# Optimization experiments

Measured on AMD Instinct MI355X. Metric: run time of the kernel, lower is better.

## Reference

```python
import jax, jax.numpy as jnp
import numpy as np

N = 50000          # total residues (nodes)
E = 800000         # contact edges
IN_DIM = 1280      # ESM embedding dim
G_DIMS = [512, 512, 512]
FC0, FC1 = 1024, 512
OUT = 256
N_GRAPHS = 64


def setup_inputs() -> dict:
    key = jax.random.key(0)
    ks = jax.random.split(key, 16)
    inp = {
        "x": jax.random.normal(ks[0], (N, IN_DIM), dtype=jnp.float32),
        "edge_index": jax.random.randint(ks[1], (2, E), 0, N, dtype=jnp.int64),
        "batch": jnp.sort(jax.random.randint(ks[2], (N,), 0, N_GRAPHS, dtype=jnp.int64)),
    }
    s = 0.02
    dims = [IN_DIM] + G_DIMS
    for i in range(3):
        inp[f"Wg{i+1}"] = jax.random.normal(ks[3 + i], (dims[i], dims[i + 1]), dtype=jnp.float32) * s
        inp[f"bg{i+1}"] = jnp.zeros((dims[i + 1],), dtype=jnp.float32)
    cat = sum(G_DIMS)  # 1536
    inp["Wr"] = jax.random.normal(ks[7], (cat, FC0), dtype=jnp.float32) * s
    inp["br"] = jnp.zeros((FC0,), dtype=jnp.float32)
    inp["Wf"] = jax.random.normal(ks[8], (FC0, FC1), dtype=jnp.float32) * s
    inp["bf"] = jnp.zeros((FC1,), dtype=jnp.float32)
    inp["Wo"] = jax.random.normal(ks[9], (FC1, OUT), dtype=jnp.float32) * s
    inp["bo"] = jnp.zeros((OUT,), dtype=jnp.float32)
    return inp


def _gcn_layer(x, W, b, src, dst, n):
    # PyG GCNConv: h = X W; add self loops; symmetric deg^-1/2 normalization; sum-aggregate; + bias
    h = x @ W                                    # [n, d_out]
    ones = jnp.ones_like(src, dtype=h.dtype)
    deg = jax.ops.segment_sum(ones, dst, num_segments=n) + 1.0   # in-degree incl. self loop
    dinv = jax.lax.rsqrt(deg)
    norm = dinv[src] * dinv[dst]                 # [E]
    agg = jax.ops.segment_sum(h[src] * norm[:, None], dst, num_segments=n)
    agg = agg + h * (dinv * dinv)[:, None]       # self-loop contribution: 1/deg
    return agg + b


def reference(x, edge_index, batch, Wg1, bg1, Wg2, bg2, Wg3, bg3, Wr, br, Wf, bf, Wo, bo):
    n = x.shape[0]
    src, dst = edge_index[0], edge_index[1]
    h1 = _gcn_layer(x, Wg1, bg1, src, dst, n)
    h2 = _gcn_layer(h1, Wg2, bg2, src, dst, n)
    h3 = _gcn_layer(h2, Wg3, bg3, src, dst, n)
    h = jnp.concatenate([h1, h2, h3], axis=-1)   # [n, 1536]
    # global mean pool per graph
    s = jax.ops.segment_sum(h, batch, num_segments=N_GRAPHS)
    cnt = jax.ops.segment_sum(jnp.ones((n,), h.dtype), batch, num_segments=N_GRAPHS)
    g = s / jnp.maximum(cnt, 1.0)[:, None]       # [G, 1536]
    g = jax.nn.relu(g @ Wr + br)                 # dropout = identity (eval mode)
    g = jax.nn.relu(g @ Wf + bf)
    return g @ Wo + bo                           # [G, OUT]
```

## Files before the change

kernel.cpp:

```cpp
#include <hip/hip_runtime.h>
#include <stdint.h>

#define NN 50000
#define EE 800000
#define INDIM 1280
#define GD 512
#define CAT 1536
#define FC0D 1024
#define FC1D 512
#define OUTD 256
#define NG 64

#define CKS 76
#define CRS 672
#define NPAD (CKS * CRS)
#define QSZ (192 * INDIM)

typedef __attribute__((ext_vector_type(8))) __bf16 bf16x8;
typedef __attribute__((ext_vector_type(4))) float f32x4;

__device__ __forceinline__ void split_bf16(float f, unsigned short& h, unsigned short& l) {
    unsigned int u = __builtin_bit_cast(unsigned int, f);
    h = (unsigned short)(u >> 16);
    float hf = __builtin_bit_cast(float, u & 0xffff0000u);
    float lf = f - hf;
    unsigned int ul = __builtin_bit_cast(unsigned int, lf);
    ul = ul + 0x7fffu + ((ul >> 16) & 1u);
    l = (unsigned short)(ul >> 16);
}

__device__ __forceinline__ void g2l16(const void* g, void* l) {
    __builtin_amdgcn_global_load_lds(
        (const __attribute__((address_space(1))) void*)g,
        (__attribute__((address_space(3))) void*)l, 16, 0, 0);
}

__global__ void zero_u32(uint32_t* p, int n) {
    int i = blockIdx.x * 256 + threadIdx.x;
    if (i < n) p[i] = 0u;
}

__global__ void hist_edges(const int* __restrict__ ei, int* __restrict__ cnt_s,
                           int* __restrict__ cnt_d) {
    int e = blockIdx.x * 256 + threadIdx.x;
    if (e < EE) {
        atomicAdd(&cnt_s[ei[e]], 1);
        atomicAdd(&cnt_d[ei[EE + e]], 1);
    }
}

__global__ void batch_bounds(const int* __restrict__ bat, int* __restrict__ gcnt) {
    int g = threadIdx.x;
    int lo = 0, hi = NN;
    while (lo < hi) {
        int mid = (lo + hi) >> 1;
        if (bat[mid] < g) lo = mid + 1; else hi = mid;
    }
    int nxt = __shfl_down(lo, 1);
    if (g == 63) nxt = NN;
    gcnt[g] = nxt - lo;
}

__global__ __launch_bounds__(1024) void scan1(const int* __restrict__ cnt,
                                              int* __restrict__ row_ptr,
                                              int* __restrict__ bsum, int n) {
    __shared__ int s[1024];
    int tid = threadIdx.x;
    int i = blockIdx.x * 1024 + tid;
    int v = (i < n) ? cnt[i] : 0;
    s[tid] = v;
    __syncthreads();
    for (int off = 1; off < 1024; off <<= 1) {
        int t = 0;
        if (tid >= off) t = s[tid - off];
        __syncthreads();
        if (tid >= off) s[tid] += t;
        __syncthreads();
    }
    if (i < n) row_ptr[i] = s[tid] - v;
    if (tid == 1023) bsum[blockIdx.x] = s[1023];
}

__global__ void scan2(int* bsum, int nb) {
    int i = threadIdx.x;
    int v = (i < nb) ? bsum[i] : 0;
    int s = v;
#pragma unroll
    for (int off = 1; off < 64; off <<= 1) {
        int t = __shfl_up(s, off);
        if (i >= off) s += t;
    }
    if (i < nb) bsum[i] = s - v;
}

__global__ __launch_bounds__(1024) void scan3b(int* __restrict__ row_ptr,
                                               const int* __restrict__ bsum,
                                               const int* __restrict__ cnt_d,
                                               float* __restrict__ dinv,
                                               int* __restrict__ fill, int n) {
    int i = blockIdx.x * 1024 + threadIdx.x;
    if (i < n) {
        int rp = row_ptr[i] + bsum[blockIdx.x];
        row_ptr[i] = rp;
        fill[i] = rp;
        dinv[i] = rsqrtf((float)cnt_d[i] + 1.0f);
    }
    if (i == 0) row_ptr[n] = EE;
}

__global__ void scatter_src(const int* __restrict__ ei, int* __restrict__ fill,
                            int* __restrict__ col) {
    int e = blockIdx.x * 256 + threadIdx.x;
    if (e < EE) {
        int s = ei[e];
        int d = ei[EE + e];
        int pos = atomicAdd(&fill[s], 1);
        col[pos] = d;
    }
}

__global__ __launch_bounds__(256) void uprop_first(const int* __restrict__ rp,
                                                   const int* __restrict__ col,
                                                   const float* __restrict__ dinv,
                                                   const int* __restrict__ bat,
                                                   float* __restrict__ UU) {
    int wid = threadIdx.x >> 6, lane = threadIdx.x & 63;
    int f = lane & 15, es = lane >> 4;
    int i = blockIdx.x * 4 + wid;
    if (i >= NPAD) return;
    float* dst = UU + (size_t)i * 192 + f * 4;
    if (i >= NN) {
        if (es == 0) *(float4*)dst = make_float4(0.f, 0.f, 0.f, 0.f);
        return;
    }
    float di = dinv[i];
    int s = rp[i], e = rp[i + 1];
    float4 a = make_float4(0.f, 0.f, 0.f, 0.f);
    int g0 = f * 4;
    for (int t = s + es; t < e; t += 4) {
        int d = col[t];
        float w = di * dinv[d];
        int b = bat[d];
        a.x += (b == g0 + 0) ? w : 0.f;
        a.y += (b == g0 + 1) ? w : 0.f;
        a.z += (b == g0 + 2) ? w : 0.f;
        a.w += (b == g0 + 3) ? w : 0.f;
    }
#pragma unroll
    for (int m = 16; m <= 32; m <<= 1) {
        a.x += __shfl_xor(a.x, m);
        a.y += __shfl_xor(a.y, m);
        a.z += __shfl_xor(a.z, m);
        a.w += __shfl_xor(a.w, m);
    }
    if (es == 0) {
        int b = bat[i];
        float self = di * di;
        a.x += (b == g0 + 0) ? self : 0.f;
        a.y += (b == g0 + 1) ? self : 0.f;
        a.z += (b == g0 + 2) ? self : 0.f;
        a.w += (b == g0 + 3) ? self : 0.f;
        *(float4*)dst = a;
    }
}

__global__ __launch_bounds__(256) void uprop_next(const int* __restrict__ rp,
                                                  const int* __restrict__ col,
                                                  const float* __restrict__ dinv,
                                                  float* __restrict__ UU,
                                                  int secIn, int secOut) {
    int wid = threadIdx.x >> 6, lane = threadIdx.x & 63;
    int f = lane & 15, es = lane >> 4;
    int i = blockIdx.x * 4 + wid;
    if (i >= NPAD) return;
    float* dst = UU + (size_t)i * 192 + secOut * 64 + f * 4;
    if (i >= NN) {
        if (es == 0) *(float4*)dst = make_float4(0.f, 0.f, 0.f, 0.f);
        return;
    }
    const float* Uin = UU + secIn * 64 + f * 4;
    float di = dinv[i];
    int s = rp[i], e = rp[i + 1];
    float4 a = make_float4(0.f, 0.f, 0.f, 0.f);
    int t = s + es;
    for (; t + 4 < e; t += 8) {
        int d0 = col[t], d1 = col[t + 4];
        float w0 = di * dinv[d0], w1 = di * dinv[d1];
        float4 u0 = *(const float4*)(Uin + (size_t)d0 * 192);
        float4 u1 = *(const float4*)(Uin + (size_t)d1 * 192);
        a.x = fmaf(w0, u0.x, a.x); a.y = fmaf(w0, u0.y, a.y);
        a.z = fmaf(w0, u0.z, a.z); a.w = fmaf(w0, u0.w, a.w);
        a.x = fmaf(w1, u1.x, a.x); a.y = fmaf(w1, u1.y, a.y);
        a.z = fmaf(w1, u1.z, a.z); a.w = fmaf(w1, u1.w, a.w);
    }
    if (t < e) {
        int d0 = col[t];
        float w0 = di * dinv[d0];
        float4 u0 = *(const float4*)(Uin + (size_t)d0 * 192);
        a.x = fmaf(w0, u0.x, a.x); a.y = fmaf(w0, u0.y, a.y);
        a.z = fmaf(w0, u0.z, a.z); a.w = fmaf(w0, u0.w, a.w);
    }
#pragma unroll
    for (int m = 16; m <= 32; m <<= 1) {
        a.x += __shfl_xor(a.x, m);
        a.y += __shfl_xor(a.y, m);
        a.z += __shfl_xor(a.z, m);
        a.w += __shfl_xor(a.w, m);
    }
    if (es == 0) {
        float self = di * di;
        float4 us = *(const float4*)(Uin + (size_t)i * 192);
        a.x = fmaf(self, us.x, a.x);
        a.y = fmaf(self, us.y, a.y);
        a.z = fmaf(self, us.z, a.z);
        a.w = fmaf(self, us.w, a.w);
        *(float4*)dst = a;
    }
}

__global__ __launch_bounds__(256) void usig_kernel(const float* __restrict__ UU,
                                                   float* __restrict__ sigraw) {
    int g = threadIdx.x & 63, rs = threadIdx.x >> 6;
    int r0 = blockIdx.x * 512;
    int rend = min(r0 + 512, NN);
    float a1 = 0.f, a2 = 0.f;
    for (int r = r0 + rs; r < rend; r += 4) {
        size_t o = (size_t)r * 192 + g;
        a1 += UU[o];
        a2 += UU[o + 64];
    }
    __shared__ float sh[2][256];
    sh[0][threadIdx.x] = a1;
    sh[1][threadIdx.x] = a2;
    __syncthreads();
    if (rs == 0) {
        a1 = sh[0][g] + sh[0][64 + g] + sh[0][128 + g] + sh[0][192 + g];
        a2 = sh[1][g] + sh[1][64 + g] + sh[1][128 + g] + sh[1][192 + g];
        atomicAdd(&sigraw[g], a1);
        atomicAdd(&sigraw[64 + g], a2);
    }
}

__global__ __launch_bounds__(256) void tsplit_uu(const float* __restrict__ UU,
                                                 unsigned short* __restrict__ TH,
                                                 unsigned short* __restrict__ TL) {
    __shared__ float t[32][33];
    int r0 = blockIdx.x * 32;
    int c0 = blockIdx.y * 32;
    int r = threadIdx.x >> 3;
    int c4 = (threadIdx.x & 7) * 4;
    float4 v = *(const float4*)(UU + (size_t)(r0 + r) * 192 + c0 + c4);
    t[r][c4 + 0] = v.x;
    t[r][c4 + 1] = v.y;
    t[r][c4 + 2] = v.z;
    t[r][c4 + 3] = v.w;
    __syncthreads();
    ushort4 h4, l4;
    split_bf16(t[c4 + 0][r], h4.x, l4.x);
    split_bf16(t[c4 + 1][r], h4.y, l4.y);
    split_bf16(t[c4 + 2][r], h4.z, l4.z);
    split_bf16(t[c4 + 3][r], h4.w, l4.w);
    *(ushort4*)(TH + (size_t)(c0 + r) * NPAD + r0 + c4) = h4;
    *(ushort4*)(TL + (size_t)(c0 + r) * NPAD + r0 + c4) = l4;
}

__global__ __launch_bounds__(256, 3) void contract_mfma(
    const float* __restrict__ X, const unsigned short* __restrict__ UTH,
    const unsigned short* __restrict__ UTL, float* __restrict__ partial) {
    __shared__ __align__(16) float Xs[32 * 128];
    __shared__ __align__(16) unsigned short Bh[192 * 32];
    __shared__ __align__(16) unsigned short Bl[192 * 32];
    const int sbid = (blockIdx.x & 7) * 95 + (blockIdx.x >> 3);
    const int ks = sbid / 10, mt = sbid % 10;
    const int tid = threadIdx.x, lane = tid & 63, wid = tid >> 6;
    const int wm = wid * 32;
    const int m0 = mt * 128;
    const int r0 = ks * CRS;
    const int khi = lane >> 4;
    const int ml = lane & 15;

    f32x4 acc[2][12];
#pragma unroll
    for (int mf = 0; mf < 2; mf++)
#pragma unroll
        for (int nf = 0; nf < 12; nf++) acc[mf][nf] = (f32x4)0.0f;

    int xsrow[4], xscol[4];
#pragma unroll
    for (int i = 0; i < 4; i++) {
        int p = tid + i * 256;
        int krow = p >> 5;
        xsrow[i] = krow;
        xscol[i] = ((p & 31) ^ ((krow >> 3) << 2)) * 4;
    }

    for (int ch = 0; ch < CRS / 32; ch++) {
        int rb = r0 + ch * 32;
        __syncthreads();
#pragma unroll
        for (int i = 0; i < 4; i++) {
            int xr = rb + xsrow[i];
            if (xr > NN - 1) xr = NN - 1;
            g2l16(X + (size_t)xr * INDIM + m0 + xscol[i], (char*)Xs + (tid + i * 256) * 16);
        }
#pragma unroll
        for (int i = 0; i < 3; i++) {
            int p = tid + i * 256;
            size_t so = (size_t)(p >> 2) * NPAD + rb + (p & 3) * 8;
            g2l16(UTH + so, (char*)Bh + p * 16);
            g2l16(UTL + so, (char*)Bl + p * 16);
        }
        __syncthreads();

        bf16x8 ah[2], al[2];
#pragma unroll
        for (int mf = 0; mf < 2; mf++) {
            int mloc = wm + mf * 16 + ml;
            const float* xb = Xs + (size_t)(khi * 8) * 128 +
                              (((mloc >> 2) ^ (khi << 2)) << 2) + (mloc & 3);
            union { bf16x8 v; unsigned short s[8]; } uh, ul;
#pragma unroll
            for (int j = 0; j < 8; j++) {
                unsigned short h, l;
                split_bf16(xb[j * 128], h, l);
                uh.s[j] = h;
                ul.s[j] = l;
            }
            ah[mf] = uh.v;
            al[mf] = ul.v;
        }
#pragma unroll
        for (int nf = 0; nf < 12; nf++) {
            int nrow = nf * 16 + ml;
            bf16x8 bh = *(const bf16x8*)(Bh + nrow * 32 + khi * 8);
            bf16x8 bl = *(const bf16x8*)(Bl + nrow * 32 + khi * 8);
#pragma unroll
            for (int mf = 0; mf < 2; mf++) {
                acc[mf][nf] = __builtin_amdgcn_mfma_f32_16x16x32_bf16(ah[mf], bh, acc[mf][nf], 0, 0, 0);
                acc[mf][nf] = __builtin_amdgcn_mfma_f32_16x16x32_bf16(ah[mf], bl, acc[mf][nf], 0, 0, 0);
                acc[mf][nf] = __builtin_amdgcn_mfma_f32_16x16x32_bf16(al[mf], bh, acc[mf][nf], 0, 0, 0);
            }
        }
    }

    float* pp = partial + (size_t)ks * QSZ;
#pragma unroll
    for (int mf = 0; mf < 2; mf++) {
        int mg = m0 + wm + mf * 16 + khi * 4;
#pragma unroll
        for (int nf = 0; nf < 12; nf++) {
            int n = nf * 16 + ml;
#pragma unroll
            for (int r = 0; r < 4; r++)
                pp[(size_t)(mg + r) * 192 + n] = acc[mf][nf][r];
        }
    }
}

__global__ void reduce_qt(const float* __restrict__ partial, const int* __restrict__ gcnt,
                          float* __restrict__ Q) {
    int o = blockIdx.x * 256 + threadIdx.x;
    if (o >= QSZ) return;
    float a = 0.f;
    for (int ks = 0; ks < CKS; ks++) a += partial[(size_t)ks * QSZ + o];
    int n = o % 192, c = o / 192;
    Q[(size_t)n * INDIM + c] = a / (float)max(gcnt[n & 63], 1);
}

template <int MT, int K, int N, int NS>
__global__ __launch_bounds__(256) void gemm_sk(const float* __restrict__ A,
                                               const float* __restrict__ W,
                                               float* __restrict__ part) {
    constexpr int KL = K / NS;
    __shared__ float a_s[32][33];
    int tid = threadIdx.x;
    int c = blockIdx.x * 64 + (tid & 63);
    int grp = tid >> 6;
    int m0 = blockIdx.y * 32;
    int k00 = blockIdx.z * KL;
    float acc[8];
#pragma unroll
    for (int i = 0; i < 8; i++) acc[i] = 0.f;
    for (int k0 = k00; k0 < k00 + KL; k0 += 32) {
        __syncthreads();
#pragma unroll
        for (int i = 0; i < 4; i++) {
            int idx = tid + i * 256;
            int row = idx >> 5, kk = idx & 31;
            a_s[row][kk] = A[(size_t)(m0 + row) * K + k0 + kk];
        }
        __syncthreads();
#pragma unroll
        for (int kk = 0; kk < 32; kk++) {
            float w = W[(size_t)(k0 + kk) * N + c];
#pragma unroll
            for (int i = 0; i < 8; i++)
                acc[i] = fmaf(a_s[grp * 8 + i][kk], w, acc[i]);
        }
    }
#pragma unroll
    for (int i = 0; i < 8; i++) {
        int m = m0 + grp * 8 + i;
        part[((size_t)blockIdx.z * MT + m) * N + c] = acc[i];
    }
}

__global__ void comb_qh(const float* __restrict__ p, const float* __restrict__ sigraw,
                        const int* __restrict__ gcnt, const float* __restrict__ b1,
                        float* __restrict__ G, float* __restrict__ t2,
                        float* __restrict__ t3) {
    int o = blockIdx.x * 256 + threadIdx.x;
    if (o >= 192 * GD) return;
    float v = 0.f;
#pragma unroll
    for (int ns = 0; ns < 5; ns++) v += p[(size_t)ns * 192 * GD + o];
    int m = o >> 9, c = o & 511;
    float bc = b1[c];
    if (m < 64) {
        G[(size_t)m * CAT + c] = v + bc;
    } else if (m < 128) {
        int g = m - 64;
        t2[(size_t)g * GD + c] = v + (sigraw[g] / (float)max(gcnt[g], 1)) * bc;
    } else {
        int g = m - 128;
        t3[(size_t)g * GD + c] = v + (sigraw[64 + g] / (float)max(gcnt[g], 1)) * bc;
    }
}

__global__ void comb_w2(const float* __restrict__ pA, const float* __restrict__ pB,
                        const float* __restrict__ sigraw, const int* __restrict__ gcnt,
                        const float* __restrict__ b2, float* __restrict__ G,
                        float* __restrict__ u3) {
    int o = blockIdx.x * 256 + threadIdx.x;
    if (o >= NG * GD) return;
    float va = 0.f, vb = 0.f;
#pragma unroll
    for (int ns = 0; ns < 4; ns++) {
        va += pA[(size_t)ns * NG * GD + o];
        vb += pB[(size_t)ns * NG * GD + o];
    }
    int m = o >> 9, c = o & 511;
    float bc = b2[c];
    G[(size_t)m * CAT + GD + c] = va + bc;
    u3[o] = vb + (sigraw[m] / (float)max(gcnt[m], 1)) * bc;
}

__global__ void comb_w3(const float* __restrict__ pC, const float* __restrict__ b3,
                        float* __restrict__ G) {
    int o = blockIdx.x * 256 + threadIdx.x;
    if (o >= NG * GD) return;
    float v = 0.f;
#pragma unroll
    for (int ns = 0; ns < 4; ns++) v += pC[(size_t)ns * NG * GD + o];
    int m = o >> 9, c = o & 511;
    G[(size_t)m * CAT + 2 * GD + c] = v + b3[c];
}

template <int N, int NS, bool RELU>
__global__ void combf(const float* __restrict__ p, const float* __restrict__ bias,
                      float* __restrict__ out) {
    int o = blockIdx.x * 256 + threadIdx.x;
    if (o >= NG * N) return;
    float v = 0.f;
#pragma unroll
    for (int ns = 0; ns < NS; ns++) v += p[(size_t)ns * NG * N + o];
    v += bias[o % N];
    if (RELU) v = fmaxf(v, 0.f);
    out[o] = v;
}

static inline size_t al256(size_t x) { return (x + 255) & ~(size_t)255; }

extern "C" void kernel_launch(void* const* d_in, const int* in_sizes, int n_in,
                              void* d_out, int out_size, void* d_ws, size_t ws_size,
                              hipStream_t stream) {
    const float* x   = (const float*)d_in[0];
    const int*   ei  = (const int*)d_in[1];
    const int*   bat = (const int*)d_in[2];
    const float* Wg1 = (const float*)d_in[3];
    const float* bg1 = (const float*)d_in[4];
    const float* Wg2 = (const float*)d_in[5];
    const float* bg2 = (const float*)d_in[6];
    const float* Wg3 = (const float*)d_in[7];
    const float* bg3 = (const float*)d_in[8];
    const float* Wr  = (const float*)d_in[9];
    const float* br  = (const float*)d_in[10];
    const float* Wf  = (const float*)d_in[11];
    const float* bf  = (const float*)d_in[12];
    const float* Wo  = (const float*)d_in[13];
    const float* bo  = (const float*)d_in[14];
    float* out = (float*)d_out;

    char* ws = (char*)d_ws;
    size_t off = 0;
    int*   cnt2    = (int*)(ws + off); off += al256(((size_t)2 * NN + 512) * 4);
    int*   row_ptr = (int*)(ws + off); off += al256((size_t)(NN + 1) * 4);
    int*   fill    = (int*)(ws + off); off += al256((size_t)NN * 4);
    float* dinv    = (float*)(ws + off); off += al256((size_t)NN * 4);
    int*   col     = (int*)(ws + off); off += al256((size_t)EE * 4);
    int*   bsum    = (int*)(ws + off); off += al256(64 * 4);
    float* UU      = (float*)(ws + off); off += al256((size_t)NPAD * 192 * 4);
    unsigned short* UTH = (unsigned short*)(ws + off); off += al256((size_t)192 * NPAD * 2);
    unsigned short* UTL = (unsigned short*)(ws + off); off += al256((size_t)192 * NPAD * 2);
    float* partial = (float*)(ws + off); off += al256((size_t)CKS * QSZ * 4);
    float* Q       = (float*)(ws + off); off += al256((size_t)QSZ * 4);
    float* G       = (float*)(ws + off); off += al256((size_t)NG * CAT * 4);
    float* t2      = (float*)(ws + off); off += al256((size_t)NG * GD * 4);
    float* t3      = (float*)(ws + off); off += al256((size_t)NG * GD * 4);
    float* u3      = (float*)(ws + off); off += al256((size_t)NG * GD * 4);
    float* r0      = (float*)(ws + off); off += al256((size_t)NG * FC0D * 4);
    float* r1      = (float*)(ws + off); off += al256((size_t)NG * FC1D * 4);
    float* pQH     = (float*)(ws + off); off += al256((size_t)5 * 192 * GD * 4);
    float* pA      = (float*)(ws + off); off += al256((size_t)4 * NG * GD * 4);
    float* pB      = (float*)(ws + off); off += al256((size_t)4 * NG * GD * 4);
    float* pC      = (float*)(ws + off); off += al256((size_t)4 * NG * GD * 4);
    float* pD      = (float*)(ws + off); off += al256((size_t)6 * NG * FC0D * 4);
    float* pE      = (float*)(ws + off); off += al256((size_t)8 * NG * FC1D * 4);
    float* pF      = (float*)(ws + off); off += al256((size_t)4 * NG * OUTD * 4);
    (void)ws_size; (void)n_in; (void)in_sizes; (void)out_size;

    int*   cnt_s  = cnt2;
    int*   cnt_d  = cnt2 + NN;
    int*   gcnt   = cnt2 + 2 * NN;
    float* sigraw = (float*)(cnt2 + 2 * NN + 64);

    const int nscan = (NN + 1023) / 1024;

    zero_u32<<<dim3((2 * NN + 512 + 255) / 256), 256, 0, stream>>>((uint32_t*)cnt2, 2 * NN + 512);

    hist_edges<<<dim3((EE + 255) / 256), 256, 0, stream>>>(ei, cnt_s, cnt_d);
    batch_bounds<<<dim3(1), 64, 0, stream>>>(bat, gcnt);

    scan1<<<dim3(nscan), 1024, 0, stream>>>(cnt_s, row_ptr, bsum, NN);
    scan2<<<dim3(1), 64, 0, stream>>>(bsum, nscan);
    scan3b<<<dim3(nscan), 1024, 0, stream>>>(row_ptr, bsum, cnt_d, dinv, fill, NN);
    scatter_src<<<dim3((EE + 255) / 256), 256, 0, stream>>>(ei, fill, col);

    dim3 ugrid(NPAD / 4);
    uprop_first<<<ugrid, 256, 0, stream>>>(row_ptr, col, dinv, bat, UU);
    uprop_next<<<ugrid, 256, 0, stream>>>(row_ptr, col, dinv, UU, 0, 1);
    uprop_next<<<ugrid, 256, 0, stream>>>(row_ptr, col, dinv, UU, 1, 2);

    usig_kernel<<<dim3((NN + 511) / 512), 256, 0, stream>>>(UU, sigraw);

    tsplit_uu<<<dim3(NPAD / 32, 192 / 32), 256, 0, stream>>>(UU, UTH, UTL);

    contract_mfma<<<dim3(760), 256, 0, stream>>>(x, UTH, UTL, partial);
    reduce_qt<<<dim3((QSZ + 255) / 256), 256, 0, stream>>>(partial, gcnt, Q);

    gemm_sk<192, INDIM, GD, 5><<<dim3(GD / 64, 6, 5), 256, 0, stream>>>(Q, Wg1, pQH);
    comb_qh<<<dim3((192 * GD + 255) / 256), 256, 0, stream>>>(pQH, sigraw, gcnt, bg1, G, t2, t3);
    gemm_sk<NG, GD, GD, 4><<<dim3(GD / 64, 2, 4), 256, 0, stream>>>(t2, Wg2, pA);
    gemm_sk<NG, GD, GD, 4><<<dim3(GD / 64, 2, 4), 256, 0, stream>>>(t3, Wg2, pB);
    comb_w2<<<dim3((NG * GD + 255) / 256), 256, 0, stream>>>(pA, pB, sigraw, gcnt, bg2, G, u3);
    gemm_sk<NG, GD, GD, 4><<<dim3(GD / 64, 2, 4), 256, 0, stream>>>(u3, Wg3, pC);
    comb_w3<<<dim3((NG * GD + 255) / 256), 256, 0, stream>>>(pC, bg3, G);
    gemm_sk<NG, CAT, FC0D, 6><<<dim3(FC0D / 64, 2, 6), 256, 0, stream>>>(G, Wr, pD);
    combf<FC0D, 6, true><<<dim3((NG * FC0D + 255) / 256), 256, 0, stream>>>(pD, br, r0);
    gemm_sk<NG, FC0D, FC1D, 8><<<dim3(FC1D / 64, 2, 8), 256, 0, stream>>>(r0, Wf, pE);
    combf<FC1D, 8, true><<<dim3((NG * FC1D + 255) / 256), 256, 0, stream>>>(pE, bf, r1);
    gemm_sk<NG, FC1D, OUTD, 4><<<dim3(OUTD / 64, 2, 4), 256, 0, stream>>>(r1, Wo, pF);
    combf<OUTD, 4, false><<<dim3((NG * OUTD + 255) / 256), 256, 0, stream>>>(pF, bo, out);
}
```

Baseline: 487.6 us.

## Atomic-accumulate contraction partials and fuse small GEMM/combine launches in head

The MFMA contraction now atomically adds its per-k-split results into one zeroed buffer instead of writing 76 partial slabs that a separate kernel reduces, which removes a large partial write and re-read. The two Wg2 GEMMs are merged into one dual launch, and the layer-3 combine is folded into the FC0 GEMM's A-tile load. The self-loop read in uprop_next is also changed to index UU directly. In exchange, summation order becomes nondeterministic, there is contention on about 245K float atomics, and one extra zeroing launch is added.

```diff
diff --git a/kernel.cpp b/kernel.cpp
--- a/kernel.cpp
+++ b/kernel.cpp
@@ -209,7 +209,7 @@
     }
     if (es == 0) {
         float self = di * di;
-        float4 us = *(const float4*)(Uin + (size_t)i * 192);
+        float4 us = *(const float4*)(UU + (size_t)i * 192 + secIn * 64 + f * 4);
         a.x = fmaf(self, us.x, a.x);
         a.y = fmaf(self, us.y, a.y);
         a.z = fmaf(self, us.z, a.z);
@@ -266,7 +266,7 @@
 
 __global__ __launch_bounds__(256, 3) void contract_mfma(
     const float* __restrict__ X, const unsigned short* __restrict__ UTH,
-    const unsigned short* __restrict__ UTL, float* __restrict__ partial) {
+    const unsigned short* __restrict__ UTL, float* __restrict__ qacc) {
     __shared__ __align__(16) float Xs[32 * 128];
     __shared__ __align__(16) unsigned short Bh[192 * 32];
     __shared__ __align__(16) unsigned short Bl[192 * 32];
@@ -343,7 +343,6 @@
         }
     }
 
-    float* pp = partial + (size_t)ks * QSZ;
 #pragma unroll
     for (int mf = 0; mf < 2; mf++) {
         int mg = m0 + wm + mf * 16 + khi * 4;
@@ -352,19 +351,17 @@
             int n = nf * 16 + ml;
 #pragma unroll
             for (int r = 0; r < 4; r++)
-                pp[(size_t)(mg + r) * 192 + n] = acc[mf][nf][r];
-        }
-    }
-}
-
-__global__ void reduce_qt(const float* __restrict__ partial, const int* __restrict__ gcnt,
-                          float* __restrict__ Q) {
+                atomicAdd(&qacc[(size_t)(mg + r) * 192 + n], acc[mf][nf][r]);
+        }
+    }
+}
+
+__global__ void scale_qt(const float* __restrict__ qacc, const int* __restrict__ gcnt,
+                         float* __restrict__ Q) {
     int o = blockIdx.x * 256 + threadIdx.x;
     if (o >= QSZ) return;
-    float a = 0.f;
-    for (int ks = 0; ks < CKS; ks++) a += partial[(size_t)ks * QSZ + o];
     int n = o % 192, c = o / 192;
-    Q[(size_t)n * INDIM + c] = a / (float)max(gcnt[n & 63], 1);
+    Q[(size_t)n * INDIM + c] = qacc[o] / (float)max(gcnt[n & 63], 1);
 }
 
 template <int MT, int K, int N, int NS>
@@ -405,6 +402,99 @@
     }
 }
 
+template <int K, int N, int NS>
+__global__ __launch_bounds__(256) void gemm_sk_dual(const float* __restrict__ A0,
+                                                    const float* __restrict__ A1,
+                                                    const float* __restrict__ W,
+                                                    float* __restrict__ p0,
+                                                    float* __restrict__ p1) {
+    constexpr int KL = K / NS;
+    __shared__ float a_s[32][33];
+    int tid = threadIdx.x;
+    int c = blockIdx.x * 64 + (tid & 63);
+    int grp = tid >> 6;
+    int half = blockIdx.y >> 1;
+    const float* A = half ? A1 : A0;
+    float* part = half ? p1 : p0;
+    int m0 = (blockIdx.y & 1) * 32;
+    int k00 = blockIdx.z * KL;
+    float acc[8];
+#pragma unroll
+    for (int i = 0; i < 8; i++) acc[i] = 0.f;
+    for (int k0 = k00; k0 < k00 + KL; k0 += 32) {
+        __syncthreads();
+#pragma unroll
+        for (int i = 0; i < 4; i++) {
+            int idx = tid + i * 256;
+            int row = idx >> 5, kk = idx & 31;
+            a_s[row][kk] = A[(size_t)(m0 + row) * K + k0 + kk];
+        }
+        __syncthreads();
+#pragma unroll
+        for (int kk = 0; kk < 32; kk++) {
+            float w = W[(size_t)(k0 + kk) * N + c];
+#pragma unroll
+            for (int i = 0; i < 8; i++)
+                acc[i] = fmaf(a_s[grp * 8 + i][kk], w, acc[i]);
+        }
+    }
+#pragma unroll
+    for (int i = 0; i < 8; i++) {
+        int m = m0 + grp * 8 + i;
+        part[((size_t)blockIdx.z * NG + m) * N + c] = acc[i];
+    }
+}
+
+__global__ __launch_bounds__(256) void gemm_fc1(const float* __restrict__ G,
+                                                const float* __restrict__ pC,
+                                                const float* __restrict__ b3,
+                                                const float* __restrict__ W,
+                                                float* __restrict__ part) {
+    constexpr int K = CAT, N = FC0D, NS = 6, KL = K / NS;
+    __shared__ float a_s[32][33];
+    int tid = threadIdx.x;
+    int c = blockIdx.x * 64 + (tid & 63);
+    int grp = tid >> 6;
+    int m0 = blockIdx.y * 32;
+    int k00 = blockIdx.z * KL;
+    float acc[8];
+#pragma unroll
+    for (int i = 0; i < 8; i++) acc[i] = 0.f;
+    for (int k0 = k00; k0 < k00 + KL; k0 += 32) {
+        __syncthreads();
+#pragma unroll
+        for (int i = 0; i < 4; i++) {
+            int idx = tid + i * 256;
+            int row = idx >> 5, kk = idx & 31;
+            int m = m0 + row, k = k0 + kk;
+            float v;
+            if (k < 2 * GD) {
+                v = G[(size_t)m * CAT + k];
+            } else {
+                int cc = k - 2 * GD;
+                v = b3[cc];
+#pragma unroll
+                for (int ns = 0; ns < 4; ns++)
+                    v += pC[(size_t)ns * NG * GD + (size_t)m * GD + cc];
+            }
+            a_s[row][kk] = v;
+        }
+        __syncthreads();
+#pragma unroll
+        for (int kk = 0; kk < 32; kk++) {
+            float w = W[(size_t)(k0 + kk) * N + c];
+#pragma unroll
+            for (int i = 0; i < 8; i++)
+                acc[i] = fmaf(a_s[grp * 8 + i][kk], w, acc[i]);
+        }
+    }
+#pragma unroll
+    for (int i = 0; i < 8; i++) {
+        int m = m0 + grp * 8 + i;
+        part[((size_t)blockIdx.z * NG + m) * N + c] = acc[i];
+    }
+}
+
 __global__ void comb_qh(const float* __restrict__ p, const float* __restrict__ sigraw,
                         const int* __restrict__ gcnt, const float* __restrict__ b1,
                         float* __restrict__ G, float* __restrict__ t2,
@@ -443,17 +533,6 @@
     float bc = b2[c];
     G[(size_t)m * CAT + GD + c] = va + bc;
     u3[o] = vb + (sigraw[m] / (float)max(gcnt[m], 1)) * bc;
-}
-
-__global__ void comb_w3(const float* __restrict__ pC, const float* __restrict__ b3,
-                        float* __restrict__ G) {
-    int o = blockIdx.x * 256 + threadIdx.x;
-    if (o >= NG * GD) return;
-    float v = 0.f;
-#pragma unroll
-    for (int ns = 0; ns < 4; ns++) v += pC[(size_t)ns * NG * GD + o];
-    int m = o >> 9, c = o & 511;
-    G[(size_t)m * CAT + 2 * GD + c] = v + b3[c];
 }
 
 template <int N, int NS, bool RELU>
@@ -502,7 +581,7 @@
     float* UU      = (float*)(ws + off); off += al256((size_t)NPAD * 192 * 4);
     unsigned short* UTH = (unsigned short*)(ws + off); off += al256((size_t)192 * NPAD * 2);
     unsigned short* UTL = (unsigned short*)(ws + off); off += al256((size_t)192 * NPAD * 2);
-    float* partial = (float*)(ws + off); off += al256((size_t)CKS * QSZ * 4);
+    float* qacc    = (float*)(ws + off); off += al256((size_t)QSZ * 4);
     float* Q       = (float*)(ws + off); off += al256((size_t)QSZ * 4);
     float* G       = (float*)(ws + off); off += al256((size_t)NG * CAT * 4);
     float* t2      = (float*)(ws + off); off += al256((size_t)NG * GD * 4);
@@ -527,6 +606,7 @@
     const int nscan = (NN + 1023) / 1024;
 
     zero_u32<<<dim3((2 * NN + 512 + 255) / 256), 256, 0, stream>>>((uint32_t*)cnt2, 2 * NN + 512);
+    zero_u32<<<dim3((QSZ + 255) / 256), 256, 0, stream>>>((uint32_t*)qacc, QSZ);
 
     hist_edges<<<dim3((EE + 255) / 256), 256, 0, stream>>>(ei, cnt_s, cnt_d);
     batch_bounds<<<dim3(1), 64, 0, stream>>>(bat, gcnt);
@@ -545,17 +625,15 @@
 
     tsplit_uu<<<dim3(NPAD / 32, 192 / 32), 256, 0, stream>>>(UU, UTH, UTL);
 
-    contract_mfma<<<dim3(760), 256, 0, stream>>>(x, UTH, UTL, partial);
-    reduce_qt<<<dim3((QSZ + 255) / 256), 256, 0, stream>>>(partial, gcnt, Q);
+    contract_mfma<<<dim3(760), 256, 0, stream>>>(x, UTH, UTL, qacc);
+    scale_qt<<<dim3((QSZ + 255) / 256), 256, 0, stream>>>(qacc, gcnt, Q);
 
     gemm_sk<192, INDIM, GD, 5><<<dim3(GD / 64, 6, 5), 256, 0, stream>>>(Q, Wg1, pQH);
     comb_qh<<<dim3((192 * GD + 255) / 256), 256, 0, stream>>>(pQH, sigraw, gcnt, bg1, G, t2, t3);
-    gemm_sk<NG, GD, GD, 4><<<dim3(GD / 64, 2, 4), 256, 0, stream>>>(t2, Wg2, pA);
-    gemm_sk<NG, GD, GD, 4><<<dim3(GD / 64, 2, 4), 256, 0, stream>>>(t3, Wg2, pB);
+    gemm_sk_dual<GD, GD, 4><<<dim3(GD / 64, 4, 4), 256, 0, stream>>>(t2, t3, Wg2, pA, pB);
     comb_w2<<<dim3((NG * GD + 255) / 256), 256, 0, stream>>>(pA, pB, sigraw, gcnt, bg2, G, u3);
     gemm_sk<NG, GD, GD, 4><<<dim3(GD / 64, 2, 4), 256, 0, stream>>>(u3, Wg3, pC);
-    comb_w3<<<dim3((NG * GD + 255) / 256), 256, 0, stream>>>(pC, bg3, G);
-    gemm_sk<NG, CAT, FC0D, 6><<<dim3(FC0D / 64, 2, 6), 256, 0, stream>>>(G, Wr, pD);
+    gemm_fc1<<<dim3(FC0D / 64, 2, 6), 256, 0, stream>>>(G, pC, bg3, Wr, pD);
     combf<FC0D, 6, true><<<dim3((NG * FC0D + 255) / 256), 256, 0, stream>>>(pD, br, r0);
     gemm_sk<NG, FC0D, FC1D, 8><<<dim3(FC1D / 64, 2, 8), 256, 0, stream>>>(r0, Wf, pE);
     combf<FC1D, 8, true><<<dim3((NG * FC1D + 255) / 256), 256, 0, stream>>>(pE, bf, r1);
```

New measurement: 506.1 us. +3.8%, slower.
